# Kernel optimization log

Hardware: AMD Instinct MI355X
Metric: run time of the kernel (lower is better)

## Reference

```python
import jax, jax.numpy as jnp
import numpy as np

D = 1024  # feature_size

def setup_inputs() -> dict:
    key = jax.random.key(0)
    ks = jax.random.split(key, 9)
    s = 1.0 / np.sqrt(D)
    inp = {"x": jax.random.normal(ks[0], (4, 2048, D), dtype=jnp.float32)}
    names = ["Wk", "Wq", "Wv", "Wo"]
    for i, n in enumerate(names):
        inp[n] = jax.random.uniform(ks[1 + 2 * i], (D, D), dtype=jnp.float32, minval=-s, maxval=s)
        inp["b" + n[1]] = jax.random.uniform(ks[2 + 2 * i], (D,), dtype=jnp.float32, minval=-s, maxval=s)
    return inp

def reference(x, Wk, bk, Wq, bq, Wv, bv, Wo, bo):
    # Linear layers: x @ W.T + b (torch nn.Linear convention)
    keys = jnp.einsum('bsd,ed->bse', x, Wk) + bk
    queries = jnp.einsum('bsd,ed->bse', x, Wq) + bq
    values = jnp.einsum('bsd,ed->bse', x, Wv) + bv
    scale = 1.0 / jnp.sqrt(jnp.float32(D))
    scores = jnp.einsum('bqd,bkd->bqk', queries, keys) * scale  # [B,S,S]
    attention = jax.nn.softmax(scores, axis=-1)
    out = jnp.einsum('bqk,bkd->bqd', attention, values)
    out = jnp.einsum('bsd,ed->bse', out, Wo) + bo
    return (out, attention)
```

## Files before the change

kernel.cpp:

```cpp
#include <hip/hip_runtime.h>
#include <hip/hip_bf16.h>


typedef __attribute__((ext_vector_type(8))) _Float16 f16x8;
typedef __attribute__((ext_vector_type(4))) _Float16 f16x4;
typedef __attribute__((ext_vector_type(4))) float f32x4;

static __device__ __forceinline__ void gl_lds16(const void* g, void* s) {
  __builtin_amdgcn_global_load_lds(
      (const __attribute__((address_space(1))) void*)g,
      (__attribute__((address_space(3))) void*)s, 16, 0, 0);
}

__global__ __launch_bounds__(256) void prep(
    const float* __restrict__ x,
    const float* __restrict__ Wq, const float* __restrict__ Wk,
    const float* __restrict__ Wo, const float* __restrict__ Wv,
    const float* __restrict__ bv, const float* __restrict__ bo,
    const float* __restrict__ bq, const float* __restrict__ bk,
    _Float16* __restrict__ xh,
    _Float16* __restrict__ Wf, _Float16* __restrict__ Woh,
    _Float16* __restrict__ WvT, float* __restrict__ cpb,
    float* __restrict__ bqkv) {
  const int b = blockIdx.x;
  const int tid = threadIdx.x;
  if (b < 8192) {
    const int i = b * 256 + tid;
    float4 v = reinterpret_cast<const float4*>(x)[i];
    f16x4 r = {(_Float16)v.x, (_Float16)v.y, (_Float16)v.z, (_Float16)v.w};
    reinterpret_cast<f16x4*>(xh)[i] = r;
  } else if (b < 11264) {
    const int bb = b - 8192;
    const float* src = (bb < 1024) ? Wq : (bb < 2048) ? Wk : Wo;
    _Float16* dst = (bb < 1024) ? Wf : (bb < 2048) ? (Wf + 1048576) : Woh;
    const int i = (bb & 1023) * 256 + tid;
    float4 v = reinterpret_cast<const float4*>(src)[i];
    f16x4 r = {(_Float16)v.x, (_Float16)v.y, (_Float16)v.z, (_Float16)v.w};
    reinterpret_cast<f16x4*>(dst)[i] = r;
  } else if (b < 11520) {
    __shared__ float t[64][65];
    const int bb = b - 11264;
    const int bx = (bb & 15) * 64, by = (bb >> 4) * 64;
    const int tx = tid & 63, ty = tid >> 6;
#pragma unroll
    for (int i = 0; i < 64; i += 4)
      t[ty + i][tx] = Wv[(long)(by + ty + i) * 1024 + bx + tx];
    __syncthreads();
#pragma unroll
    for (int i = 0; i < 64; i += 4)
      WvT[(long)(bx + ty + i) * 1024 + by + tx] = (_Float16)t[tx][ty + i];
  } else if (b < 12544) {
    const int n = b - 11520;
    float s = 0.f;
    for (int d = tid; d < 1024; d += 256) s += Wo[(long)n * 1024 + d] * bv[d];
#pragma unroll
    for (int o = 32; o >= 1; o >>= 1) s += __shfl_xor(s, o);
    __shared__ float red[4];
    if ((tid & 63) == 0) red[tid >> 6] = s;
    __syncthreads();
    if (tid == 0) cpb[n] = red[0] + red[1] + red[2] + red[3] + bo[n];
  } else {
    const int i = (b - 12544) * 256 + tid;
    if (i < 3072) bqkv[i] = (i < 1024) ? bq[i] : (i < 2048) ? bk[i - 1024] : 0.f;
  }
}

template <int EPI, bool BB>
__global__ __launch_bounds__(256) void gemm128(
    const _Float16* __restrict__ A, const _Float16* __restrict__ B,
    const float* __restrict__ bias, float* __restrict__ Cf,
    _Float16* __restrict__ Ch, _Float16* __restrict__ C2,
    _Float16* __restrict__ C3,
    int M, int N, int K, long sA, long sB, long sC, float alpha, int panelW) {
  __shared__ _Float16 lds[3][2][4096];

  const unsigned gx = gridDim.x, gy = gridDim.y;
  const unsigned nwg = gx * gy * gridDim.z;
  unsigned flat = (blockIdx.z * gy + blockIdx.y) * gx + blockIdx.x;
  flat = (flat & 7) * (nwg >> 3) + (flat >> 3);
  const unsigned pb = gy * panelW;
  const long bz = flat / (gx * gy);
  const unsigned rem = flat % (gx * gy);
  const unsigned pi = rem / pb;
  const unsigned rem2 = rem % pb;
  const unsigned byi = rem2 / panelW;
  const unsigned bxi = pi * panelW + rem2 % panelW;

  const int tid = threadIdx.x;
  const int w = tid >> 6, lane = tid & 63;
  const int wr = w >> 1, wc = w & 1;
  const int lr = lane & 15, q = lane >> 4;
  const long row0 = (long)byi * 128;
  const long col0 = (long)bxi * 128;
  const int nt = K >> 5;

  const _Float16* pA = A + bz * sA;
  const _Float16* pB = BB ? (B + (row0 >> 11) * sB) : (B + bz * sB);

  f32x4 acc[4][4] = {};

  const int r0 = tid >> 2, c0 = ((tid & 3) - (r0 >> 1)) & 3;
  const int s1 = tid + 256;
  const int r1 = s1 >> 2, c1 = ((s1 & 3) - (r1 >> 1)) & 3;

  auto stage = [&](int kt) {
    if (kt >= nt) return;
    const int bf = kt % 3;
    const long gk = (long)kt * 32;
#pragma unroll
    for (int ab = 0; ab < 2; ++ab) {
      const _Float16* src = ab ? pB : pA;
      const long base = ab ? col0 : row0;
      gl_lds16(src + (base + r0) * (long)K + gk + c0 * 8, &lds[bf][ab][w << 9]);
      gl_lds16(src + (base + r1) * (long)K + gk + c1 * 8, &lds[bf][ab][2048 + (w << 9)]);
    }
  };
  auto rd = [&](int bf, int ab, int r) -> f16x8 {
    const int slot = (r << 2) + ((q + (r >> 1)) & 3);
    return *(const f16x8*)&lds[bf][ab][slot << 3];
  };

  stage(0); stage(1);
  asm volatile("s_waitcnt vmcnt(4)" ::: "memory");
  __builtin_amdgcn_s_barrier();
  __builtin_amdgcn_sched_barrier(0);

  for (int kt = 0; kt < nt; ++kt) {
    const int bf = kt % 3;
    stage(kt + 2);
    f16x8 a[4], b[4];
#pragma unroll
    for (int m = 0; m < 4; ++m) a[m] = rd(bf, 0, wr * 64 + m * 16 + lr);
#pragma unroll
    for (int n = 0; n < 4; ++n) b[n] = rd(bf, 1, wc * 64 + n * 16 + lr);
#pragma unroll
    for (int m = 0; m < 4; ++m)
#pragma unroll
      for (int n = 0; n < 4; ++n)
        acc[m][n] = __builtin_amdgcn_mfma_f32_16x16x32_f16(a[m], b[n], acc[m][n], 0, 0, 0);
    if (kt < nt - 2) asm volatile("s_waitcnt vmcnt(4)" ::: "memory");
    else             asm volatile("s_waitcnt vmcnt(0)" ::: "memory");
    __builtin_amdgcn_s_barrier();
    __builtin_amdgcn_sched_barrier(0);
  }

  if (EPI == 3 && col0 >= 2048) {
    _Float16* t = (_Float16*)&lds[0][0][0];
#pragma unroll
    for (int m = 0; m < 4; ++m)
#pragma unroll
      for (int n = 0; n < 4; ++n)
#pragma unroll
        for (int r = 0; r < 4; ++r) {
          const int rr = wr * 64 + m * 16 + q * 4 + r;
          const int cc = wc * 64 + n * 16 + lr;
          float v = acc[m][n][r] * alpha;
          if (bias) v += bias[col0 + cc];
          t[cc * 132 + rr] = (_Float16)v;
        }
    __syncthreads();
    const long b2 = row0 >> 11;
    const long s2b = row0 & 2047;
    const int n = tid >> 1, s0 = (tid & 1) * 64;
    _Float16* dst = C3 + (b2 * 1024 + (col0 - 2048) + n) * 2048 + s2b + s0;
    const _Float16* srcT = t + n * 132 + s0;
#pragma unroll
    for (int j = 0; j < 8; ++j)
      *(f16x8*)(dst + j * 8) = *(const f16x8*)(srcT + j * 8);
    return;
  }

#pragma unroll
  for (int m = 0; m < 4; ++m)
#pragma unroll
    for (int n = 0; n < 4; ++n)
#pragma unroll
      for (int r = 0; r < 4; ++r) {
        const long row = row0 + wr * 64 + m * 16 + q * 4 + r;
        const long col = col0 + wc * 64 + n * 16 + lr;
        float v = acc[m][n][r] * alpha;
        if (bias) v += bias[col];
        if (EPI == 0) {
          Cf[bz * sC + row * (long)N + col] = v;
        } else if (EPI == 1) {
          Ch[bz * sC + row * (long)N + col] = (_Float16)v;
        } else {
          if (col < 1024) Ch[row * 1024 + col] = (_Float16)v;
          else            C2[row * 1024 + (col - 1024)] = (_Float16)v;
        }
      }
}

__global__ __launch_bounds__(256) void softmax16(
    _Float16* __restrict__ Ph, float* __restrict__ attn) {
  const long row = blockIdx.x;
  _Float16* ph = Ph + row * 2048;
  float* ap = attn + row * 2048;
  const int tid = threadIdx.x;
  f16x8 v = reinterpret_cast<const f16x8*>(ph)[tid];
  float x[8];
#pragma unroll
  for (int j = 0; j < 8; ++j) x[j] = (float)v[j];
  float m = x[0];
#pragma unroll
  for (int j = 1; j < 8; ++j) m = fmaxf(m, x[j]);
#pragma unroll
  for (int o = 32; o >= 1; o >>= 1) m = fmaxf(m, __shfl_xor(m, o));
  __shared__ float red[4], red2[4];
  if ((tid & 63) == 0) red[tid >> 6] = m;
  __syncthreads();
  m = fmaxf(fmaxf(red[0], red[1]), fmaxf(red[2], red[3]));
  float s = 0.f;
#pragma unroll
  for (int j = 0; j < 8; ++j) { x[j] = expf(x[j] - m); s += x[j]; }
#pragma unroll
  for (int o = 32; o >= 1; o >>= 1) s += __shfl_xor(s, o);
  if ((tid & 63) == 0) red2[tid >> 6] = s;
  __syncthreads();
  s = red2[0] + red2[1] + red2[2] + red2[3];
  const float inv = 1.0f / s;
#pragma unroll
  for (int j = 0; j < 8; ++j) x[j] *= inv;
  reinterpret_cast<float4*>(ap)[tid * 2] = make_float4(x[0], x[1], x[2], x[3]);
  reinterpret_cast<float4*>(ap)[tid * 2 + 1] = make_float4(x[4], x[5], x[6], x[7]);
  f16x8 pv;
#pragma unroll
  for (int j = 0; j < 8; ++j) pv[j] = (_Float16)x[j];
  reinterpret_cast<f16x8*>(ph)[tid] = pv;
}

extern "C" void kernel_launch(void* const* d_in, const int* in_sizes, int n_in,
                              void* d_out, int out_size, void* d_ws, size_t ws_size,
                              hipStream_t stream) {
  const float* x  = (const float*)d_in[0];
  const float* Wk = (const float*)d_in[1];
  const float* bk = (const float*)d_in[2];
  const float* Wq = (const float*)d_in[3];
  const float* bq = (const float*)d_in[4];
  const float* Wv = (const float*)d_in[5];
  const float* bv = (const float*)d_in[6];
  const float* Wo = (const float*)d_in[7];
  const float* bo = (const float*)d_in[8];

  float* out  = (float*)d_out;
  float* attn = (float*)d_out + 8388608;

  const size_t MB = 1024 * 1024;
  unsigned char* ws = (unsigned char*)d_ws;
  _Float16* xh   = (_Float16*)(ws + 0 * MB);
  _Float16* Wf   = (_Float16*)(ws + 16 * MB);
  _Float16* Woh  = (_Float16*)(ws + 22 * MB);
  _Float16* WvT  = (_Float16*)(ws + 24 * MB);
  float*    bqkv = (float*)   (ws + 26 * MB);
  float*    cpb  = (float*)   (ws + 26 * MB + 16384);
  _Float16* Qh   = (_Float16*)(ws + 27 * MB);
  _Float16* Kh   = (_Float16*)(ws + 43 * MB);
  _Float16* Vt   = (_Float16*)(ws + 59 * MB);
  _Float16* Ph   = (_Float16*)(ws + 75 * MB);

  dim3 blk(256);
  const _Float16* nullh = nullptr;

  hipLaunchKernelGGL(prep, dim3(12556), blk, 0, stream,
                     x, Wq, Wk, Wo, Wv, bv, bo, bq, bk,
                     xh, Wf, Woh, WvT, cpb, bqkv);

  hipLaunchKernelGGL((gemm128<1, false>), dim3(8, 8, 1), blk, 0, stream,
                     Woh, WvT, (const float*)nullptr, (float*)nullptr,
                     Wf + 2097152, (_Float16*)nullh, (_Float16*)nullh,
                     1024, 1024, 1024, 0L, 0L, 0L, 1.0f, 8);
  hipLaunchKernelGGL((gemm128<3, false>), dim3(24, 64, 1), blk, 0, stream,
                     xh, Wf, bqkv, (float*)nullptr, Qh, Kh, Vt,
                     8192, 3072, 1024, 0L, 0L, 0L, 1.0f, 12);
  hipLaunchKernelGGL((gemm128<1, false>), dim3(16, 16, 4), blk, 0, stream,
                     Qh, Kh, (const float*)nullptr, (float*)nullptr, Ph,
                     (_Float16*)nullh, (_Float16*)nullh,
                     2048, 2048, 1024, 2097152L, 2097152L, 4194304L, 0.03125f, 8);
  hipLaunchKernelGGL(softmax16, dim3(8192), blk, 0, stream, Ph, attn);
  hipLaunchKernelGGL((gemm128<0, true>), dim3(8, 64, 1), blk, 0, stream,
                     Ph, Vt, cpb, out, (_Float16*)nullh, (_Float16*)nullh,
                     (_Float16*)nullh,
                     8192, 1024, 2048, 0L, 2097152L, 0L, 1.0f, 4);
}
```

Baseline: 237.1 us.

## Fold Wq·Wkᵀ into a single projection so scores use x directly

```diff
diff --git a/kernel.cpp b/kernel.cpp
--- a/kernel.cpp
+++ b/kernel.cpp
@@ -17,11 +17,9 @@
     const float* __restrict__ Wq, const float* __restrict__ Wk,
     const float* __restrict__ Wo, const float* __restrict__ Wv,
     const float* __restrict__ bv, const float* __restrict__ bo,
-    const float* __restrict__ bq, const float* __restrict__ bk,
-    _Float16* __restrict__ xh,
-    _Float16* __restrict__ Wf, _Float16* __restrict__ Woh,
-    _Float16* __restrict__ WvT, float* __restrict__ cpb,
-    float* __restrict__ bqkv) {
+    _Float16* __restrict__ xh, _Float16* __restrict__ Woh,
+    _Float16* __restrict__ WvT, _Float16* __restrict__ WqT,
+    _Float16* __restrict__ WkT, float* __restrict__ cpb) {
   const int b = blockIdx.x;
   const int tid = threadIdx.x;
   if (b < 8192) {
@@ -29,28 +27,29 @@
     float4 v = reinterpret_cast<const float4*>(x)[i];
     f16x4 r = {(_Float16)v.x, (_Float16)v.y, (_Float16)v.z, (_Float16)v.w};
     reinterpret_cast<f16x4*>(xh)[i] = r;
-  } else if (b < 11264) {
-    const int bb = b - 8192;
-    const float* src = (bb < 1024) ? Wq : (bb < 2048) ? Wk : Wo;
-    _Float16* dst = (bb < 1024) ? Wf : (bb < 2048) ? (Wf + 1048576) : Woh;
-    const int i = (bb & 1023) * 256 + tid;
-    float4 v = reinterpret_cast<const float4*>(src)[i];
+  } else if (b < 9216) {
+    const int i = (b - 8192) * 256 + tid;
+    float4 v = reinterpret_cast<const float4*>(Wo)[i];
     f16x4 r = {(_Float16)v.x, (_Float16)v.y, (_Float16)v.z, (_Float16)v.w};
-    reinterpret_cast<f16x4*>(dst)[i] = r;
-  } else if (b < 11520) {
+    reinterpret_cast<f16x4*>(Woh)[i] = r;
+  } else if (b < 9984) {
+    const int bb = b - 9216;
+    const int which = bb >> 8;
+    const float* src = which == 0 ? Wv : which == 1 ? Wq : Wk;
+    _Float16* dst = which == 0 ? WvT : which == 1 ? WqT : WkT;
     __shared__ float t[64][65];
-    const int bb = b - 11264;
-    const int bx = (bb & 15) * 64, by = (bb >> 4) * 64;
+    const int tb = bb & 255;
+    const int bx = (tb & 15) * 64, by = (tb >> 4) * 64;
     const int tx = tid & 63, ty = tid >> 6;
 #pragma unroll
     for (int i = 0; i < 64; i += 4)
-      t[ty + i][tx] = Wv[(long)(by + ty + i) * 1024 + bx + tx];
+      t[ty + i][tx] = src[(long)(by + ty + i) * 1024 + bx + tx];
     __syncthreads();
 #pragma unroll
     for (int i = 0; i < 64; i += 4)
-      WvT[(long)(bx + ty + i) * 1024 + by + tx] = (_Float16)t[tx][ty + i];
-  } else if (b < 12544) {
-    const int n = b - 11520;
+      dst[(long)(bx + ty + i) * 1024 + by + tx] = (_Float16)t[tx][ty + i];
+  } else {
+    const int n = b - 9984;
     float s = 0.f;
     for (int d = tid; d < 1024; d += 256) s += Wo[(long)n * 1024 + d] * bv[d];
 #pragma unroll
@@ -59,9 +58,57 @@
     if ((tid & 63) == 0) red[tid >> 6] = s;
     __syncthreads();
     if (tid == 0) cpb[n] = red[0] + red[1] + red[2] + red[3] + bo[n];
+  }
+}
+
+__global__ __launch_bounds__(256) void wkern(
+    const float* __restrict__ bq, const float* __restrict__ bk,
+    const _Float16* __restrict__ WkT, const _Float16* __restrict__ WqT,
+    float* __restrict__ w1, float* __restrict__ w2, float* __restrict__ c0) {
+  const int b = blockIdx.x;
+  const int tid = threadIdx.x;
+  float s = 0.f;
+  if (b < 1024) {
+    for (int e = tid; e < 1024; e += 256) s += bq[e] * (float)WkT[(long)b * 1024 + e];
+  } else if (b < 2048) {
+    const int d = b - 1024;
+    for (int e = tid; e < 1024; e += 256) s += bk[e] * (float)WqT[(long)d * 1024 + e];
   } else {
-    const int i = (b - 12544) * 256 + tid;
-    if (i < 3072) bqkv[i] = (i < 1024) ? bq[i] : (i < 2048) ? bk[i - 1024] : 0.f;
+    for (int e = tid; e < 1024; e += 256) s += bq[e] * bk[e];
+  }
+#pragma unroll
+  for (int o = 32; o >= 1; o >>= 1) s += __shfl_xor(s, o);
+  __shared__ float red[4];
+  if ((tid & 63) == 0) red[tid >> 6] = s;
+  __syncthreads();
+  if (tid == 0) {
+    const float v = red[0] + red[1] + red[2] + red[3];
+    if (b < 1024) w1[b] = v;
+    else if (b < 2048) w2[b - 1024] = v;
+    else c0[0] = v;
+  }
+}
+
+__global__ __launch_bounds__(256) void rowcol(
+    const _Float16* __restrict__ xh, const float* __restrict__ w1,
+    const float* __restrict__ w2, const float* __restrict__ c0,
+    float* __restrict__ rowb, float* __restrict__ colb) {
+  const long i = blockIdx.x;
+  const int tid = threadIdx.x;
+  f16x4 xv = reinterpret_cast<const f16x4*>(xh + i * 1024)[tid];
+  float4 a1 = reinterpret_cast<const float4*>(w1)[tid];
+  float4 a2 = reinterpret_cast<const float4*>(w2)[tid];
+  float x0 = (float)xv[0], x1 = (float)xv[1], x2 = (float)xv[2], x3 = (float)xv[3];
+  float d1 = x0 * a1.x + x1 * a1.y + x2 * a1.z + x3 * a1.w;
+  float d2 = x0 * a2.x + x1 * a2.y + x2 * a2.z + x3 * a2.w;
+#pragma unroll
+  for (int o = 32; o >= 1; o >>= 1) { d1 += __shfl_xor(d1, o); d2 += __shfl_xor(d2, o); }
+  __shared__ float r1[4], r2[4];
+  if ((tid & 63) == 0) { r1[tid >> 6] = d1; r2[tid >> 6] = d2; }
+  __syncthreads();
+  if (tid == 0) {
+    colb[i] = (r1[0] + r1[1] + r1[2] + r1[3]) * 0.03125f;
+    rowb[i] = (r2[0] + r2[1] + r2[2] + r2[3] + c0[0]) * 0.03125f;
   }
 }
 
@@ -69,8 +116,7 @@
 __global__ __launch_bounds__(256) void gemm128(
     const _Float16* __restrict__ A, const _Float16* __restrict__ B,
     const float* __restrict__ bias, float* __restrict__ Cf,
-    _Float16* __restrict__ Ch, _Float16* __restrict__ C2,
-    _Float16* __restrict__ C3,
+    _Float16* __restrict__ Ch, _Float16* __restrict__ C3,
     int M, int N, int K, long sA, long sB, long sC, float alpha, int panelW) {
   __shared__ _Float16 lds[3][2][4096];
 
@@ -99,7 +145,7 @@
 
   f32x4 acc[4][4] = {};
 
-  const int r0 = tid >> 2, c0 = ((tid & 3) - (r0 >> 1)) & 3;
+  const int r0 = tid >> 2, c0i = ((tid & 3) - (r0 >> 1)) & 3;
   const int s1 = tid + 256;
   const int r1 = s1 >> 2, c1 = ((s1 & 3) - (r1 >> 1)) & 3;
 
@@ -111,7 +157,7 @@
     for (int ab = 0; ab < 2; ++ab) {
       const _Float16* src = ab ? pB : pA;
       const long base = ab ? col0 : row0;
-      gl_lds16(src + (base + r0) * (long)K + gk + c0 * 8, &lds[bf][ab][w << 9]);
+      gl_lds16(src + (base + r0) * (long)K + gk + c0i * 8, &lds[bf][ab][w << 9]);
       gl_lds16(src + (base + r1) * (long)K + gk + c1 * 8, &lds[bf][ab][2048 + (w << 9)]);
     }
   };
@@ -144,7 +190,7 @@
     __builtin_amdgcn_sched_barrier(0);
   }
 
-  if (EPI == 3 && col0 >= 2048) {
+  if (EPI == 3 && col0 >= 1024) {
     _Float16* t = (_Float16*)&lds[0][0][0];
 #pragma unroll
     for (int m = 0; m < 4; ++m)
@@ -154,15 +200,13 @@
         for (int r = 0; r < 4; ++r) {
           const int rr = wr * 64 + m * 16 + q * 4 + r;
           const int cc = wc * 64 + n * 16 + lr;
-          float v = acc[m][n][r] * alpha;
-          if (bias) v += bias[col0 + cc];
-          t[cc * 132 + rr] = (_Float16)v;
+          t[cc * 132 + rr] = (_Float16)(acc[m][n][r] * alpha);
         }
     __syncthreads();
     const long b2 = row0 >> 11;
     const long s2b = row0 & 2047;
     const int n = tid >> 1, s0 = (tid & 1) * 64;
-    _Float16* dst = C3 + (b2 * 1024 + (col0 - 2048) + n) * 2048 + s2b + s0;
+    _Float16* dst = C3 + (b2 * 1024 + (col0 - 1024) + n) * 2048 + s2b + s0;
     const _Float16* srcT = t + n * 132 + s0;
 #pragma unroll
     for (int j = 0; j < 8; ++j)
@@ -179,14 +223,17 @@
         const long row = row0 + wr * 64 + m * 16 + q * 4 + r;
         const long col = col0 + wc * 64 + n * 16 + lr;
         float v = acc[m][n][r] * alpha;
-        if (bias) v += bias[col];
-        if (EPI == 0) {
+        if (EPI == 2) {
+          v += Cf[bz * 2048 + row] + bias[bz * 2048 + col];
+          Ch[bz * sC + row * (long)N + col] = (_Float16)v;
+        } else if (EPI == 0) {
+          if (bias) v += bias[col];
           Cf[bz * sC + row * (long)N + col] = v;
         } else if (EPI == 1) {
+          if (bias) v += bias[col];
           Ch[bz * sC + row * (long)N + col] = (_Float16)v;
         } else {
-          if (col < 1024) Ch[row * 1024 + col] = (_Float16)v;
-          else            C2[row * 1024 + (col - 1024)] = (_Float16)v;
+          Ch[row * 1024 + col] = (_Float16)v;
         }
       }
 }
@@ -249,36 +296,43 @@
   unsigned char* ws = (unsigned char*)d_ws;
   _Float16* xh   = (_Float16*)(ws + 0 * MB);
   _Float16* Wf   = (_Float16*)(ws + 16 * MB);
+  _Float16* WqT  = (_Float16*)(ws + 20 * MB);
   _Float16* Woh  = (_Float16*)(ws + 22 * MB);
   _Float16* WvT  = (_Float16*)(ws + 24 * MB);
-  float*    bqkv = (float*)   (ws + 26 * MB);
-  float*    cpb  = (float*)   (ws + 26 * MB + 16384);
-  _Float16* Qh   = (_Float16*)(ws + 27 * MB);
-  _Float16* Kh   = (_Float16*)(ws + 43 * MB);
-  _Float16* Vt   = (_Float16*)(ws + 59 * MB);
-  _Float16* Ph   = (_Float16*)(ws + 75 * MB);
+  _Float16* WkT  = (_Float16*)(ws + 26 * MB);
+  float*    rowb = (float*)   (ws + 28 * MB);
+  float*    colb = (float*)   (ws + 28 * MB + 32768);
+  float*    cpb  = (float*)   (ws + 28 * MB + 65536);
+  float*    w1   = (float*)   (ws + 28 * MB + 69632);
+  float*    w2   = (float*)   (ws + 28 * MB + 73728);
+  float*    c0s  = (float*)   (ws + 28 * MB + 77824);
+  _Float16* Y    = (_Float16*)(ws + 29 * MB);
+  _Float16* Vt   = (_Float16*)(ws + 45 * MB);
+  _Float16* Ph   = (_Float16*)(ws + 61 * MB);
 
   dim3 blk(256);
   const _Float16* nullh = nullptr;
 
-  hipLaunchKernelGGL(prep, dim3(12556), blk, 0, stream,
-                     x, Wq, Wk, Wo, Wv, bv, bo, bq, bk,
-                     xh, Wf, Woh, WvT, cpb, bqkv);
-
+  hipLaunchKernelGGL(prep, dim3(11008), blk, 0, stream,
+                     x, Wq, Wk, Wo, Wv, bv, bo, xh, Woh, WvT, WqT, WkT, cpb);
+  hipLaunchKernelGGL(wkern, dim3(2049), blk, 0, stream, bq, bk, WkT, WqT, w1, w2, c0s);
+  hipLaunchKernelGGL((gemm128<1, false>), dim3(8, 8, 1), blk, 0, stream,
+                     WkT, WqT, (const float*)nullptr, (float*)nullptr,
+                     Wf, (_Float16*)nullh,
+                     1024, 1024, 1024, 0L, 0L, 0L, 1.0f, 8);
   hipLaunchKernelGGL((gemm128<1, false>), dim3(8, 8, 1), blk, 0, stream,
                      Woh, WvT, (const float*)nullptr, (float*)nullptr,
-                     Wf + 2097152, (_Float16*)nullh, (_Float16*)nullh,
+                     Wf + 1048576, (_Float16*)nullh,
                      1024, 1024, 1024, 0L, 0L, 0L, 1.0f, 8);
-  hipLaunchKernelGGL((gemm128<3, false>), dim3(24, 64, 1), blk, 0, stream,
-                     xh, Wf, bqkv, (float*)nullptr, Qh, Kh, Vt,
-                     8192, 3072, 1024, 0L, 0L, 0L, 1.0f, 12);
-  hipLaunchKernelGGL((gemm128<1, false>), dim3(16, 16, 4), blk, 0, stream,
-                     Qh, Kh, (const float*)nullptr, (float*)nullptr, Ph,
-                     (_Float16*)nullh, (_Float16*)nullh,
+  hipLaunchKernelGGL(rowcol, dim3(8192), blk, 0, stream, xh, w1, w2, c0s, rowb, colb);
+  hipLaunchKernelGGL((gemm128<3, false>), dim3(16, 64, 1), blk, 0, stream,
+                     xh, Wf, (const float*)nullptr, (float*)nullptr, Y, Vt,
+                     8192, 2048, 1024, 0L, 0L, 0L, 1.0f, 8);
+  hipLaunchKernelGGL((gemm128<2, false>), dim3(16, 16, 4), blk, 0, stream,
+                     Y, xh, colb, rowb, Ph, (_Float16*)nullh,
                      2048, 2048, 1024, 2097152L, 2097152L, 4194304L, 0.03125f, 8);
   hipLaunchKernelGGL(softmax16, dim3(8192), blk, 0, stream, Ph, attn);
   hipLaunchKernelGGL((gemm128<0, true>), dim3(8, 64, 1), blk, 0, stream,
                      Ph, Vt, cpb, out, (_Float16*)nullh, (_Float16*)nullh,
-                     (_Float16*)nullh,
                      8192, 1024, 2048, 0L, 2097152L, 0L, 1.0f, 4);
 }
```

After: 225.5 us. -4.9%, faster.
